# Optimization experiments

Hardware: AMD Instinct MI355X
Metric: run time of the kernel (lower is better)

The kernel has to match this reference:

```python
import jax, jax.numpy as jnp
import numpy as np

B, T, DM, H, D = 4, 2048, 1024, 16, 64
INNER = H * D


def setup_inputs() -> dict:
    key = jax.random.key(0)
    ks = jax.random.split(key, 8)
    s = 0.02
    x = jax.random.normal(ks[0], (B, T, DM), dtype=jnp.float32)
    state = jnp.zeros((B, H, D, D), dtype=jnp.float32)
    Wq = jax.random.normal(ks[1], (DM, INNER), dtype=jnp.float32) * s
    Wk = jax.random.normal(ks[2], (DM, INNER), dtype=jnp.float32) * s
    Wv = jax.random.normal(ks[3], (DM, INNER), dtype=jnp.float32) * s
    Wa = jax.random.normal(ks[4], (DM, H), dtype=jnp.float32) * s
    ba = jnp.zeros((H,), dtype=jnp.float32)
    Wb = jax.random.normal(ks[5], (DM, H), dtype=jnp.float32) * s
    bb = jnp.zeros((H,), dtype=jnp.float32)  # beta_init=0.5 -> logit(0.5)=0
    Wo = jax.random.normal(ks[6], (INNER, DM), dtype=jnp.float32) * s
    return {"x": x, "state": state, "Wq": Wq, "Wk": Wk, "Wv": Wv,
            "Wa": Wa, "ba": ba, "Wb": Wb, "bb": bb, "Wo": Wo}


def reference(x, state, Wq, Wk, Wv, Wa, ba, Wb, bb, Wo):
    Bb, Tt, _ = x.shape
    Q = (x @ Wq).reshape(Bb, Tt, H, D)
    K = (x @ Wk).reshape(Bb, Tt, H, D)
    V = (x @ Wv).reshape(Bb, Tt, H, D)
    alpha = jax.nn.sigmoid(x @ Wa + ba)  # (B,T,H) forget gate
    beta = jax.nn.sigmoid(x @ Wb + bb)   # (B,T,H) write gate
    # F.normalize(p=2, dim=-1) with eps=1e-12 clamp on the norm
    K = K / jnp.maximum(jnp.linalg.norm(K, axis=-1, keepdims=True), 1e-12)

    def step(S, inp):
        qt, kt, vt, at, bt = inp  # (B,H,D),(B,H,D),(B,H,D),(B,H),(B,H)
        S = at[..., None, None] * S + bt[..., None, None] * jnp.einsum('bhi,bhj->bhij', vt, kt)
        yt = jnp.einsum('bhij,bhj->bhi', S, qt)
        return S, yt

    xs = (jnp.swapaxes(Q, 0, 1), jnp.swapaxes(K, 0, 1), jnp.swapaxes(V, 0, 1),
          jnp.swapaxes(alpha, 0, 1), jnp.swapaxes(beta, 0, 1))
    S, ys = jax.lax.scan(step, state, xs)  # ys: (T,B,H,D)
    out = jnp.swapaxes(ys, 0, 1).reshape(Bb, Tt, INNER) @ Wo
    return out, S
```

## Files before the change

### kernel.cpp

```cpp
#include <hip/hip_runtime.h>
#include <hip/hip_bf16.h>
#include <math.h>

#define B_SZ   4
#define T_LEN  2048
#define DM     1024
#define NH     16
#define DH     64
#define INNER  1024
#define NROWS  (B_SZ*T_LEN)
#define NQ     (NROWS*INNER)
#define CH     64
#define NCH    (T_LEN/CH)

typedef __bf16 bf16x8 __attribute__((ext_vector_type(8)));
typedef __bf16 bf16x4 __attribute__((ext_vector_type(4)));
typedef float  f32x4  __attribute__((ext_vector_type(4)));
typedef __attribute__((address_space(3))) void*       lds_vp;
typedef const __attribute__((address_space(1))) void* gbl_vp;

__device__ __forceinline__ int swz(int row, int col) {
    return (row << 6) + ((((col >> 3) + (row >> 2)) & 7) << 3) + (col & 7);
}

__global__ __launch_bounds__(256) void wt_cast_transpose(const float* __restrict__ Wq,
                                                         const float* __restrict__ Wk,
                                                         const float* __restrict__ Wv,
                                                         const float* __restrict__ Wo,
                                                         __bf16* __restrict__ WqT,
                                                         __bf16* __restrict__ WkT,
                                                         __bf16* __restrict__ WvT,
                                                         __bf16* __restrict__ WoT) {
    __shared__ float tile[64][65];
    const float* W;
    __bf16* WT;
    if      (blockIdx.z == 0) { W = Wq; WT = WqT; }
    else if (blockIdx.z == 1) { W = Wk; WT = WkT; }
    else if (blockIdx.z == 2) { W = Wv; WT = WvT; }
    else                      { W = Wo; WT = WoT; }

    const int k0 = blockIdx.y * 64, n0 = blockIdx.x * 64;
    const int tr  = threadIdx.x >> 4;
    const int tc4 = (threadIdx.x & 15) * 4;

#pragma unroll
    for (int r = 0; r < 4; r++) {
        const int k = tr + 16 * r;
        const float4 v = *(const float4*)(W + (size_t)(k0 + k) * DM + n0 + tc4);
        tile[k][tc4 + 0] = v.x;
        tile[k][tc4 + 1] = v.y;
        tile[k][tc4 + 2] = v.z;
        tile[k][tc4 + 3] = v.w;
    }
    __syncthreads();
#pragma unroll
    for (int r = 0; r < 4; r++) {
        const int n = tr + 16 * r;
        bf16x4 o;
#pragma unroll
        for (int j = 0; j < 4; j++) o[j] = (__bf16)tile[tc4 + j][n];
        *(bf16x4*)(WT + (size_t)(n0 + n) * DM + k0 + tc4) = o;
    }
}

#define STAGE_STRIDE 24576
#define B_BASE 16384

template <typename CT>
__device__ __forceinline__ void gemm_pipe_body(const __bf16* __restrict__ A,
                                               const __bf16* __restrict__ BT,
                                               CT* __restrict__ C,
                                               int m0, int n0bt, int n0c) {
    __shared__ __align__(16) char lds[3 * STAGE_STRIDE];

    const int tid  = threadIdx.x;
    const int wid  = tid >> 6;
    const int lane = tid & 63;
    const int wm = wid >> 1;
    const int wn = wid & 1;
    const int frow = lane & 15, quad = lane >> 4;

    int offA[8], offB[4];
#pragma unroll
    for (int i = 0; i < 8; ++i) {
        const int ra = wm * 128 + i * 16 + frow;
        offA[i] = ra * 64 + ((quad ^ ((ra >> 1) & 3)) << 4);
    }
#pragma unroll
    for (int j = 0; j < 4; ++j) {
        const int rb = wn * 64 + j * 16 + frow;
        offB[j] = B_BASE + rb * 64 + ((quad ^ ((rb >> 1) & 3)) << 4);
    }

    const int lr = lane >> 2;
    const int cs = ((lane & 3) ^ ((lane >> 3) & 3)) << 3;
    const __bf16* gA[4];
#pragma unroll
    for (int q = 0; q < 4; ++q)
        gA[q] = A + (size_t)(m0 + wid * 64 + q * 16 + lr) * 1024 + cs;
    const __bf16* gB[2];
#pragma unroll
    for (int q = 0; q < 2; ++q)
        gB[q] = BT + (size_t)(n0bt + wid * 32 + q * 16 + lr) * 1024 + cs;

#define STG(t_, b_) do {                                                           \
        _Pragma("unroll")                                                          \
        for (int q_ = 0; q_ < 4; ++q_)                                             \
            __builtin_amdgcn_global_load_lds((gbl_vp)(gA[q_] + (size_t)(t_) * 32), \
                (lds_vp)(lds + (b_) * STAGE_STRIDE + (wid * 64 + q_ * 16) * 64),   \
                16, 0, 0);                                                         \
        _Pragma("unroll")                                                          \
        for (int q_ = 0; q_ < 2; ++q_)                                             \
            __builtin_amdgcn_global_load_lds((gbl_vp)(gB[q_] + (size_t)(t_) * 32), \
                (lds_vp)(lds + (b_) * STAGE_STRIDE + B_BASE + (wid * 32 + q_ * 16) * 64), \
                16, 0, 0);                                                         \
    } while (0)

#define VM6 asm volatile("s_waitcnt vmcnt(6)" ::: "memory")
#define VM0 asm volatile("s_waitcnt vmcnt(0)" ::: "memory")

    f32x4 acc[8][4];
#pragma unroll
    for (int i = 0; i < 8; i++)
#pragma unroll
        for (int j = 0; j < 4; j++) acc[i][j] = (f32x4)0.f;

    STG(0, 0); STG(1, 1);
    VM6;
    asm volatile("s_barrier" ::: "memory");

#define PH(b_, STG_STMT, VM_STMT)                                                  \
    {                                                                              \
        const char* Sb_ = lds + (b_) * STAGE_STRIDE;                               \
        bf16x8 af_[8], bfr_[4];                                                    \
        _Pragma("unroll")                                                          \
        for (int i_ = 0; i_ < 8; ++i_) af_[i_]  = *(const bf16x8*)(Sb_ + offA[i_]);\
        _Pragma("unroll")                                                          \
        for (int j_ = 0; j_ < 4; ++j_) bfr_[j_] = *(const bf16x8*)(Sb_ + offB[j_]);\
        STG_STMT;                                                                  \
        asm volatile("s_barrier" ::: "memory");                                    \
        asm volatile("s_waitcnt lgkmcnt(0)" ::: "memory");                         \
        __builtin_amdgcn_sched_barrier(0);                                         \
        __builtin_amdgcn_s_setprio(1);                                             \
        _Pragma("unroll")                                                          \
        for (int mi_ = 0; mi_ < 8; ++mi_)                                          \
            _Pragma("unroll")                                                      \
            for (int nj_ = 0; nj_ < 4; ++nj_)                                      \
                acc[mi_][nj_] = __builtin_amdgcn_mfma_f32_16x16x32_bf16(           \
                    af_[mi_], bfr_[nj_], acc[mi_][nj_], 0, 0, 0);                  \
        __builtin_amdgcn_s_setprio(0);                                             \
        VM_STMT;                                                                   \
        asm volatile("s_barrier" ::: "memory");                                    \
    }

    for (int u = 0; u < 10; ++u) {
        const int p = 3 * u;
        PH(0, STG(p + 2, 2), VM6);
        PH(1, STG(p + 3, 0), VM6);
        PH(2, STG(p + 4, 1), VM6);
    }
    PH(0, , VM0);
    PH(1, , );

#undef PH
#undef STG
#undef VM6
#undef VM0

    const int cr = quad * 4, cc = frow;
#pragma unroll
    for (int mi = 0; mi < 8; ++mi) {
#pragma unroll
        for (int nj = 0; nj < 4; ++nj) {
            CT* Cp = C + (size_t)(m0 + wm * 128 + mi * 16 + cr) * 1024
                       + n0c + wn * 64 + nj * 16 + cc;
#pragma unroll
            for (int r = 0; r < 4; r++) Cp[(size_t)r * 1024] = (CT)acc[mi][nj][r];
        }
    }
}

__global__ __launch_bounds__(256, 2) void qkv_gemm_8ph(const __bf16* __restrict__ xb,
                                                       const __bf16* __restrict__ BTall,
                                                       __bf16* __restrict__ QKV) {
    const int id = blockIdx.x;
    const int wg = (id & 7) * 96 + (id >> 3);
    const int mt = wg / 24, nt = wg % 24;
    const int mat = nt >> 3;
    gemm_pipe_body<__bf16>(xb, BTall, QKV + (size_t)mat * NQ,
                           mt * 256, nt * 128, (nt & 7) * 128);
}

__global__ __launch_bounds__(256, 2) void out_gemm_8ph(const __bf16* __restrict__ Yb,
                                                       const __bf16* __restrict__ WoT,
                                                       float* __restrict__ Cout) {
    const int id = blockIdx.x;
    const int wg = (id & 7) * 32 + (id >> 3);
    const int mt = wg >> 3, nt = wg & 7;
    gemm_pipe_body<float>(Yb, WoT, Cout, mt * 256, nt * 128, nt * 128);
}

#define WGS  1032
#define LAS2 72
__global__ __launch_bounds__(256) void gates_fused(const float* __restrict__ x,
                                                   const float* __restrict__ Wa,
                                                   const float* __restrict__ ba,
                                                   const float* __restrict__ Wb,
                                                   const float* __restrict__ bb,
                                                   float* __restrict__ AlphaT,
                                                   float* __restrict__ BetaT,
                                                   __bf16* __restrict__ xb) {
    __shared__ __align__(16) __bf16 lWg[32 * WGS];
    __shared__ __align__(16) __bf16 lA[32 * LAS2];

    const int tid = threadIdx.x;
    const int wid = tid >> 6, lane = tid & 63;
    const int quad = lane >> 4, frow = lane & 15;
    const int rh = wid >> 1, ct = wid & 1;
    const int m0 = blockIdx.x * 32;

    {
        const int kbase = tid * 4;
#pragma unroll
        for (int j = 0; j < 4; j++) {
            const int k = kbase + j;
            const float4* war = (const float4*)(Wa + (size_t)k * NH);
            const float4* wbr = (const float4*)(Wb + (size_t)k * NH);
#pragma unroll
            for (int q = 0; q < 4; q++) {
                const float4 a = war[q], bq = wbr[q];
                lWg[(q * 4 + 0) * WGS + k] = (__bf16)a.x;
                lWg[(q * 4 + 1) * WGS + k] = (__bf16)a.y;
                lWg[(q * 4 + 2) * WGS + k] = (__bf16)a.z;
                lWg[(q * 4 + 3) * WGS + k] = (__bf16)a.w;
                lWg[(16 + q * 4 + 0) * WGS + k] = (__bf16)bq.x;
                lWg[(16 + q * 4 + 1) * WGS + k] = (__bf16)bq.y;
                lWg[(16 + q * 4 + 2) * WGS + k] = (__bf16)bq.z;
                lWg[(16 + q * 4 + 3) * WGS + k] = (__bf16)bq.w;
            }
        }
    }
    const float bias = (ct == 0) ? ba[frow] : bb[frow];

    const int rrow = tid >> 3;
    const int rk   = (tid & 7) * 8;
    const float* xrow = x + (size_t)(m0 + rrow) * DM + rk;
    float4 c0 = *(const float4*)(xrow + 0);
    float4 c1 = *(const float4*)(xrow + 4);

    f32x4 acc = (f32x4)0.f;

    for (int k0 = 0; k0 < DM; k0 += 64) {
        __syncthreads();
        bf16x8 xv;
        xv[0] = (__bf16)c0.x; xv[1] = (__bf16)c0.y; xv[2] = (__bf16)c0.z; xv[3] = (__bf16)c0.w;
        xv[4] = (__bf16)c1.x; xv[5] = (__bf16)c1.y; xv[6] = (__bf16)c1.z; xv[7] = (__bf16)c1.w;
        *(bf16x8*)&lA[rrow * LAS2 + rk] = xv;
        *(bf16x8*)(xb + (size_t)(m0 + rrow) * DM + k0 + rk) = xv;
        if (k0 + 64 < DM) {
            c0 = *(const float4*)(xrow + k0 + 64);
            c1 = *(const float4*)(xrow + k0 + 68);
        }
        __syncthreads();
#pragma unroll
        for (int ks = 0; ks < 2; ks++) {
            const bf16x8 af = *(const bf16x8*)&lA[(rh * 16 + frow) * LAS2 + ks * 32 + quad * 8];
            const bf16x8 bf = *(const bf16x8*)&lWg[(ct * 16 + frow) * WGS + k0 + ks * 32 + quad * 8];
            acc = __builtin_amdgcn_mfma_f32_16x16x32_bf16(af, bf, acc, 0, 0, 0);
        }
    }

    float* dst = (ct == 0) ? AlphaT : BetaT;
#pragma unroll
    for (int r = 0; r < 4; r++) {
        const int row = m0 + rh * 16 + quad * 4 + r;
        const float s = acc[r] + bias;
        dst[(size_t)frow * NROWS + row] = 1.f / (1.f + __expf(-s));
    }
}

__global__ __launch_bounds__(256) void chunk_ds(const __bf16* __restrict__ Q,
                                                const __bf16* __restrict__ K,
                                                __bf16* __restrict__ V,
                                                const float* __restrict__ AlphaT,
                                                const float* __restrict__ BetaT,
                                                float* __restrict__ Dec,
                                                float* __restrict__ DS,
                                                float* __restrict__ ExpT) {
    __shared__ __align__(16) __bf16 Qb[64 * 64];
    __shared__ __align__(16) __bf16 Kb[64 * 64];
    __shared__ __align__(16) __bf16 KTs[64 * 64];
    __shared__ __align__(16) __bf16 VTb[64 * 64];
    __shared__ __align__(16) __bf16 Ab[64 * 64];
    __shared__ float sla[64], sb[64], swd[64];

    const int blk = blockIdx.x;
    const int c = blk & 31, h = (blk >> 5) & 15, b = blk >> 9;
    const int t0 = c * CH;
    const int tid = threadIdx.x;
    const int wid = tid >> 6, lane = tid & 63;
    const size_t rowbase = ((size_t)(b * T_LEN + t0) * NH + h) * DH;

    const int srow = tid >> 3;
    const int scol = (tid & 7) * 8;
    bf16x8 q8[2], k8[2], v8[2];
#pragma unroll
    for (int r = 0; r < 2; r++) {
        const size_t g = rowbase + (size_t)(srow + 32 * r) * INNER + scol;
        q8[r] = *(const bf16x8*)(Q + g);
        k8[r] = *(const bf16x8*)(K + g);
        v8[r] = *(const bf16x8*)(V + g);
    }

    if (tid < 64) {
        const int t = tid;
        const size_t gaT = (size_t)h * NROWS + b * T_LEN + t0 + t;
        const float a  = AlphaT[gaT];
        const float bt = BetaT[gaT];
        float xx = logf(a);
#pragma unroll
        for (int off = 1; off < 64; off <<= 1) {
            const float y = __shfl_up(xx, off, 64);
            if (t >= off) xx += y;
        }
        const float la63 = __shfl(xx, 63, 64);
        sla[t] = xx;
        sb[t]  = bt;
        swd[t] = bt * __expf(la63 - xx);
        ExpT[gaT] = __expf(xx);
        if (t == 63) Dec[(size_t)(b * NH + h) * NCH + c] = __expf(la63);
    }
    __syncthreads();

#pragma unroll
    for (int r = 0; r < 2; r++) {
        const int row = srow + 32 * r;
        float kf[8];
        float ss = 0.f;
#pragma unroll
        for (int j = 0; j < 8; j++) { kf[j] = (float)k8[r][j]; ss += kf[j] * kf[j]; }
        ss += __shfl_xor(ss, 1, 64);
        ss += __shfl_xor(ss, 2, 64);
        ss += __shfl_xor(ss, 4, 64);
        const float scale = 1.f / fmaxf(sqrtf(ss), 1e-12f);
        const float w = swd[row];
        bf16x8 kn8;
#pragma unroll
        for (int j = 0; j < 8; j++) {
            const float kn = kf[j] * scale;
            kn8[j] = (__bf16)kn;
            KTs[swz(scol + j, row)] = (__bf16)(w * kn);
            VTb[swz(scol + j, row)] = v8[r][j];
        }
        *(bf16x8*)&Qb[swz(row, scol)] = q8[r];
        *(bf16x8*)&Kb[swz(row, scol)] = kn8;
    }
    __syncthreads();

    const int quad = lane >> 4;
    const int frow = lane & 15;
    const int tw = wid * 16;

    f32x4 accG[4];
#pragma unroll
    for (int i = 0; i < 4; i++) accG[i] = (f32x4)0.f;
#pragma unroll
    for (int ks = 0; ks < 2; ks++) {
        const int ko = quad * 8 + 32 * ks;
        const bf16x8 aq = *(const bf16x8*)&Qb[swz(tw + frow, ko)];
#pragma unroll
        for (int st = 0; st < 4; st++) {
            const bf16x8 bk = *(const bf16x8*)&Kb[swz(st * 16 + frow, ko)];
            accG[st] = __builtin_amdgcn_mfma_f32_16x16x32_bf16(aq, bk, accG[st], 0, 0, 0);
        }
    }
#pragma unroll
    for (int st = 0; st < 4; st++) {
#pragma unroll
        for (int r = 0; r < 4; r++) {
            const int t = tw + quad * 4 + r;
            const int s = st * 16 + frow;
            const float av = (s <= t) ? __expf(sla[t] - sla[s]) * sb[s] * accG[st][r] : 0.f;
            Ab[swz(t, s)] = (__bf16)av;
        }
    }
    __syncthreads();

    f32x4 accY[4], accD[4];
#pragma unroll
    for (int i = 0; i < 4; i++) { accY[i] = (f32x4)0.f; accD[i] = (f32x4)0.f; }
#pragma unroll
    for (int ks = 0; ks < 2; ks++) {
        const int ko = quad * 8 + 32 * ks;
        const bf16x8 aA = *(const bf16x8*)&Ab[swz(tw + frow, ko)];
        const bf16x8 aK = *(const bf16x8*)&KTs[swz(tw + frow, ko)];
#pragma unroll
        for (int jt = 0; jt < 4; jt++) {
            const bf16x8 bv = *(const bf16x8*)&VTb[swz(jt * 16 + frow, ko)];
            accY[jt] = __builtin_amdgcn_mfma_f32_16x16x32_bf16(aA, bv, accY[jt], 0, 0, 0);
            accD[jt] = __builtin_amdgcn_mfma_f32_16x16x32_bf16(aK, bv, accD[jt], 0, 0, 0);
        }
    }
#pragma unroll
    for (int jt = 0; jt < 4; jt++) {
#pragma unroll
        for (int r = 0; r < 4; r++) {
            const int row = tw + quad * 4 + r;
            const size_t g = rowbase + (size_t)row * INNER + jt * 16 + frow;
            V[g]  = (__bf16)accY[jt][r];
            DS[g] = accD[jt][r];
        }
    }
}

__global__ __launch_bounds__(256) void state_y(const __bf16* __restrict__ Q,
                                               const float* __restrict__ DS,
                                               const float* __restrict__ Dec,
                                               const float* __restrict__ ExpT,
                                               const float* __restrict__ state_in,
                                               float* __restrict__ state_out,
                                               __bf16* __restrict__ Yb) {
    const int blk = blockIdx.x;
    const int b = blk >> 6, h = (blk >> 2) & 15, iq = blk & 3;
    const int tid = threadIdx.x;
    const int wid = tid >> 6, lane = tid & 63;
    const int frow = lane & 15, quad = lane >> 4;
    const int tw = wid * 16;
    const int i = iq * 16 + frow;

    float S[2][8];
    {
        const float* st = state_in + ((size_t)((b * NH + h) * DH) + i) * DH;
#pragma unroll
        for (int ks = 0; ks < 2; ks++) {
            const int j0 = 32 * ks + quad * 8;
            const float4 a = *(const float4*)(st + j0);
            const float4 d = *(const float4*)(st + j0 + 4);
            S[ks][0] = a.x; S[ks][1] = a.y; S[ks][2] = a.z; S[ks][3] = a.w;
            S[ks][4] = d.x; S[ks][5] = d.y; S[ks][6] = d.z; S[ks][7] = d.w;
        }
    }

    const size_t bh = (size_t)(b * NH + h);
#pragma unroll 2
    for (int c = 0; c < NCH; c++) {
        const int t0 = c * CH;
        const size_t rowbase = ((size_t)(b * T_LEN + t0) * NH + h) * DH;
        const float decay = Dec[bh * NCH + c];

        const bf16x8 aq0 = *(const bf16x8*)(Q + rowbase + (size_t)(tw + frow) * INNER + quad * 8);
        const bf16x8 aq1 = *(const bf16x8*)(Q + rowbase + (size_t)(tw + frow) * INNER + 32 + quad * 8);

        float ds[2][8];
#pragma unroll
        for (int ks = 0; ks < 2; ks++) {
            const int j0 = 32 * ks + quad * 8;
#pragma unroll
            for (int e = 0; e < 8; e++)
                ds[ks][e] = DS[rowbase + (size_t)(j0 + e) * INNER + i];
        }

        bf16x8 bs0, bs1;
#pragma unroll
        for (int e = 0; e < 8; e++) { bs0[e] = (__bf16)S[0][e]; bs1[e] = (__bf16)S[1][e]; }

        f32x4 acc = (f32x4)0.f;
        acc = __builtin_amdgcn_mfma_f32_16x16x32_bf16(aq0, bs0, acc, 0, 0, 0);
        acc = __builtin_amdgcn_mfma_f32_16x16x32_bf16(aq1, bs1, acc, 0, 0, 0);

#pragma unroll
        for (int ks = 0; ks < 2; ks++)
#pragma unroll
            for (int e = 0; e < 8; e++)
                S[ks][e] = decay * S[ks][e] + ds[ks][e];

#pragma unroll
        for (int r = 0; r < 4; r++) {
            const int t = tw + quad * 4 + r;
            const float ee = ExpT[(size_t)h * NROWS + b * T_LEN + t0 + t];
            __bf16* yp = Yb + rowbase + (size_t)t * INNER + i;
            *yp = (__bf16)(ee * acc[r] + (float)*yp);
        }
    }

    float* so = state_out + ((size_t)((b * NH + h) * DH) + i) * DH;
#pragma unroll
    for (int ks = 0; ks < 2; ks++) {
        const int j0 = 32 * ks + quad * 8;
        const float4 v0 = {S[ks][0], S[ks][1], S[ks][2], S[ks][3]};
        const float4 v1 = {S[ks][4], S[ks][5], S[ks][6], S[ks][7]};
        *(float4*)(so + j0)     = v0;
        *(float4*)(so + j0 + 4) = v1;
    }
}

extern "C" void kernel_launch(void* const* d_in, const int* in_sizes, int n_in,
                              void* d_out, int out_size, void* d_ws, size_t ws_size,
                              hipStream_t stream) {
    const float* x     = (const float*)d_in[0];
    const float* state = (const float*)d_in[1];
    const float* Wq    = (const float*)d_in[2];
    const float* Wk    = (const float*)d_in[3];
    const float* Wv    = (const float*)d_in[4];
    const float* Wa    = (const float*)d_in[5];
    const float* ba    = (const float*)d_in[6];
    const float* Wb    = (const float*)d_in[7];
    const float* bb    = (const float*)d_in[8];
    const float* Wo    = (const float*)d_in[9];

    __bf16* Qb    = (__bf16*)d_ws;
    __bf16* Kbf   = Qb + (size_t)NQ;
    __bf16* Vbf   = Kbf + (size_t)NQ;
    float*  DS    = (float*)(Vbf + (size_t)NQ);
    float*  AlphaT= DS + (size_t)NQ;
    float*  BetaT = AlphaT + (size_t)NROWS * NH;
    float*  ExpT  = BetaT + (size_t)NROWS * NH;
    float*  Dec   = ExpT + (size_t)NROWS * NH;
    __bf16* xb    = (__bf16*)(Dec + (size_t)B_SZ * NH * NCH);
    __bf16* WqT   = xb + (size_t)NQ;
    __bf16* WkT   = WqT + (size_t)DM * INNER;
    __bf16* WvT   = WkT + (size_t)DM * INNER;
    __bf16* WoT   = WvT + (size_t)DM * INNER;

    float* out  = (float*)d_out;
    float* Sout = out + (size_t)NQ;

    wt_cast_transpose<<<dim3(16, 16, 4), 256, 0, stream>>>(Wq, Wk, Wv, Wo,
                                                           WqT, WkT, WvT, WoT);
    gates_fused<<<NROWS / 32, 256, 0, stream>>>(x, Wa, ba, Wb, bb,
                                                AlphaT, BetaT, xb);
    qkv_gemm_8ph<<<768, 256, 0, stream>>>(xb, WqT, Qb);
    chunk_ds<<<B_SZ * NH * NCH, 256, 0, stream>>>(Qb, Kbf, Vbf, AlphaT, BetaT,
                                                  Dec, DS, ExpT);
    state_y<<<B_SZ * NH * 4, 256, 0, stream>>>(Qb, DS, Dec, ExpT, state,
                                               Sout, Vbf);
    out_gemm_8ph<<<256, 256, 0, stream>>>(Vbf, WoT, out);
}
```

Before: 256.2 us.

## Use 128x128 tiled output GEMM, reuse LDS in chunk_ds, XCD-remap state_y blocks

Adds a new 128x128-tile, three-stage pipelined GEMM body for the output projection and launches it on 512 blocks instead of 256 with 256x128 tiles, so more of the GPU's compute units are busy. In chunk_ds the A matrix now reuses the Q buffer in LDS, with an extra barrier, which cuts shared memory use and may raise occupancy. state_y remaps block indices so that blocks for the same batch-head land on the same XCD, to improve L2 locality. The smaller tiles reduce operand reuse, and the extra barrier adds a synchronisation point.

After: 238.9 us. 1.07x faster.

```diff
diff --git a/kernel.cpp b/kernel.cpp
--- a/kernel.cpp
+++ b/kernel.cpp
@@ -180,6 +180,119 @@
     }
 }
 
+#define STAGE2 16384
+#define B_BASE2 8192
+
+__device__ __forceinline__ void gemm_pipe128_body(const __bf16* __restrict__ A,
+                                                  const __bf16* __restrict__ BT,
+                                                  float* __restrict__ C,
+                                                  int m0, int n0bt, int n0c) {
+    __shared__ __align__(16) char lds[3 * STAGE2];
+
+    const int tid  = threadIdx.x;
+    const int wid  = tid >> 6;
+    const int lane = tid & 63;
+    const int wm = wid >> 1;
+    const int wn = wid & 1;
+    const int frow = lane & 15, quad = lane >> 4;
+
+    int offA[4], offB[4];
+#pragma unroll
+    for (int j = 0; j < 4; ++j) {
+        const int ra = wm * 64 + j * 16 + frow;
+        offA[j] = ra * 64 + ((quad ^ ((ra >> 1) & 3)) << 4);
+        const int rb = wn * 64 + j * 16 + frow;
+        offB[j] = B_BASE2 + rb * 64 + ((quad ^ ((rb >> 1) & 3)) << 4);
+    }
+
+    const int lr = lane >> 2;
+    const int cs = ((lane & 3) ^ ((lane >> 3) & 3)) << 3;
+    const __bf16* gA[2];
+    const __bf16* gB[2];
+#pragma unroll
+    for (int q = 0; q < 2; ++q) {
+        gA[q] = A  + (size_t)(m0 + wid * 32 + q * 16 + lr) * 1024 + cs;
+        gB[q] = BT + (size_t)(n0bt + wid * 32 + q * 16 + lr) * 1024 + cs;
+    }
+
+#define STG2(t_, b_) do {                                                          \
+        _Pragma("unroll")                                                          \
+        for (int q_ = 0; q_ < 2; ++q_)                                             \
+            __builtin_amdgcn_global_load_lds((gbl_vp)(gA[q_] + (size_t)(t_) * 32), \
+                (lds_vp)(lds + (b_) * STAGE2 + (wid * 32 + q_ * 16) * 64),         \
+                16, 0, 0);                                                         \
+        _Pragma("unroll")                                                          \
+        for (int q_ = 0; q_ < 2; ++q_)                                             \
+            __builtin_amdgcn_global_load_lds((gbl_vp)(gB[q_] + (size_t)(t_) * 32), \
+                (lds_vp)(lds + (b_) * STAGE2 + B_BASE2 + (wid * 32 + q_ * 16) * 64), \
+                16, 0, 0);                                                         \
+    } while (0)
+
+#define VM4 asm volatile("s_waitcnt vmcnt(4)" ::: "memory")
+#define VM0 asm volatile("s_waitcnt vmcnt(0)" ::: "memory")
+
+    f32x4 acc[4][4];
+#pragma unroll
+    for (int i = 0; i < 4; i++)
+#pragma unroll
+        for (int j = 0; j < 4; j++) acc[i][j] = (f32x4)0.f;
+
+    STG2(0, 0); STG2(1, 1);
+    VM4;
+    asm volatile("s_barrier" ::: "memory");
+
+#define PH2(b_, STG_STMT, VM_STMT)                                                 \
+    {                                                                              \
+        const char* Sb_ = lds + (b_) * STAGE2;                                     \
+        bf16x8 af_[4], bfr_[4];                                                    \
+        _Pragma("unroll")                                                          \
+        for (int j_ = 0; j_ < 4; ++j_) {                                           \
+            af_[j_]  = *(const bf16x8*)(Sb_ + offA[j_]);                           \
+            bfr_[j_] = *(const bf16x8*)(Sb_ + offB[j_]);                           \
+        }                                                                          \
+        STG_STMT;                                                                  \
+        asm volatile("s_barrier" ::: "memory");                                    \
+        asm volatile("s_waitcnt lgkmcnt(0)" ::: "memory");                         \
+        __builtin_amdgcn_sched_barrier(0);                                         \
+        __builtin_amdgcn_s_setprio(1);                                             \
+        _Pragma("unroll")                                                          \
+        for (int mi_ = 0; mi_ < 4; ++mi_)                                          \
+            _Pragma("unroll")                                                      \
+            for (int nj_ = 0; nj_ < 4; ++nj_)                                      \
+                acc[mi_][nj_] = __builtin_amdgcn_mfma_f32_16x16x32_bf16(           \
+                    af_[mi_], bfr_[nj_], acc[mi_][nj_], 0, 0, 0);                  \
+        __builtin_amdgcn_s_setprio(0);                                             \
+        VM_STMT;                                                                   \
+        asm volatile("s_barrier" ::: "memory");                                    \
+    }
+
+    for (int u = 0; u < 10; ++u) {
+        const int p = 3 * u;
+        PH2(0, STG2(p + 2, 2), VM4);
+        PH2(1, STG2(p + 3, 0), VM4);
+        PH2(2, STG2(p + 4, 1), VM4);
+    }
+    PH2(0, , VM0);
+    PH2(1, , );
+
+#undef PH2
+#undef STG2
+#undef VM4
+#undef VM0
+
+    const int cr = quad * 4, cc = frow;
+#pragma unroll
+    for (int mi = 0; mi < 4; ++mi) {
+#pragma unroll
+        for (int nj = 0; nj < 4; ++nj) {
+            float* Cp = C + (size_t)(m0 + wm * 64 + mi * 16 + cr) * 1024
+                          + n0c + wn * 64 + nj * 16 + cc;
+#pragma unroll
+            for (int r = 0; r < 4; r++) Cp[(size_t)r * 1024] = acc[mi][nj][r];
+        }
+    }
+}
+
 __global__ __launch_bounds__(256, 2) void qkv_gemm_8ph(const __bf16* __restrict__ xb,
                                                        const __bf16* __restrict__ BTall,
                                                        __bf16* __restrict__ QKV) {
@@ -191,13 +304,13 @@
                            mt * 256, nt * 128, (nt & 7) * 128);
 }
 
-__global__ __launch_bounds__(256, 2) void out_gemm_8ph(const __bf16* __restrict__ Yb,
+__global__ __launch_bounds__(256, 2) void out_gemm_128(const __bf16* __restrict__ Yb,
                                                        const __bf16* __restrict__ WoT,
                                                        float* __restrict__ Cout) {
     const int id = blockIdx.x;
-    const int wg = (id & 7) * 32 + (id >> 3);
+    const int wg = (id & 7) * 64 + (id >> 3);
     const int mt = wg >> 3, nt = wg & 7;
-    gemm_pipe_body<float>(Yb, WoT, Cout, mt * 256, nt * 128, nt * 128);
+    gemm_pipe128_body(Yb, WoT, Cout, mt * 128, nt * 128, nt * 128);
 }
 
 #define WGS  1032
@@ -291,8 +404,8 @@
     __shared__ __align__(16) __bf16 Kb[64 * 64];
     __shared__ __align__(16) __bf16 KTs[64 * 64];
     __shared__ __align__(16) __bf16 VTb[64 * 64];
-    __shared__ __align__(16) __bf16 Ab[64 * 64];
     __shared__ float sla[64], sb[64], swd[64];
+    __bf16* Ab = Qb;
 
     const int blk = blockIdx.x;
     const int c = blk & 31, h = (blk >> 5) & 15, b = blk >> 9;
@@ -374,6 +487,7 @@
             accG[st] = __builtin_amdgcn_mfma_f32_16x16x32_bf16(aq, bk, accG[st], 0, 0, 0);
         }
     }
+    __syncthreads();
 #pragma unroll
     for (int st = 0; st < 4; st++) {
 #pragma unroll
@@ -420,8 +534,11 @@
                                                const float* __restrict__ state_in,
                                                float* __restrict__ state_out,
                                                __bf16* __restrict__ Yb) {
-    const int blk = blockIdx.x;
-    const int b = blk >> 6, h = (blk >> 2) & 15, iq = blk & 3;
+    const int p = blockIdx.x;
+    const int xcd = p & 7, idx = p >> 3;
+    const int bh = xcd * 8 + (idx >> 2);
+    const int iq = idx & 3;
+    const int b = bh >> 4, h = bh & 15;
     const int tid = threadIdx.x;
     const int wid = tid >> 6, lane = tid & 63;
     const int frow = lane & 15, quad = lane >> 4;
@@ -441,12 +558,12 @@
         }
     }
 
-    const size_t bh = (size_t)(b * NH + h);
+    const size_t bhs = (size_t)(b * NH + h);
 #pragma unroll 2
     for (int c = 0; c < NCH; c++) {
         const int t0 = c * CH;
         const size_t rowbase = ((size_t)(b * T_LEN + t0) * NH + h) * DH;
-        const float decay = Dec[bh * NCH + c];
+        const float decay = Dec[bhs * NCH + c];
 
         const bf16x8 aq0 = *(const bf16x8*)(Q + rowbase + (size_t)(tw + frow) * INNER + quad * 8);
         const bf16x8 aq1 = *(const bf16x8*)(Q + rowbase + (size_t)(tw + frow) * INNER + 32 + quad * 8);
@@ -534,5 +651,5 @@
                                                   Dec, DS, ExpT);
     state_y<<<B_SZ * NH * 4, 256, 0, stream>>>(Qb, DS, Dec, ExpT, state,
                                                Sout, Vbf);
-    out_gemm_8ph<<<256, 256, 0, stream>>>(Vbf, WoT, out);
-}
+    out_gemm_128<<<512, 256, 0, stream>>>(Vbf, WoT, out);
+}
```
